# Performance work log

Hardware: AMD Instinct MI355X
Metric: run time of the kernel (lower is better)

Reference implementation:

```python
import jax, jax.numpy as jnp
import numpy as np

N_NODES = 10000
N_EDGES = 320000
IN_DIM = 512
HID = 64
H0 = 8
OUT = 64
H1 = 1
NEG_SLOPE = 0.2


def gat_layer(h, src, dst, W, attn_l, attn_r, n_nodes, activation=None):
    # h: (N, F_in); W: (F_in, H*D); attn_l/attn_r: (H, D)
    H, D = attn_l.shape
    feat = (h @ W).reshape(n_nodes, H, D)            # (N, H, D)
    el = jnp.einsum('nhd,hd->nh', feat, attn_l)      # (N, H)
    er = jnp.einsum('nhd,hd->nh', feat, attn_r)      # (N, H)
    e = jax.nn.leaky_relu(el[src] + er[dst], NEG_SLOPE)  # (E, H)
    # edge softmax over incoming edges of each destination node
    m = jax.ops.segment_max(e, dst, num_segments=n_nodes)   # (N, H), -inf for isolated
    m = jnp.where(jnp.isfinite(m), m, 0.0)
    ex = jnp.exp(e - m[dst])                         # (E, H)
    s = jax.ops.segment_sum(ex, dst, num_segments=n_nodes)  # (N, H)
    alpha = ex / s[dst]                              # (E, H)
    # weighted aggregation: out[dst] += alpha * feat[src]
    out = jax.ops.segment_sum(alpha[:, :, None] * feat[src], dst,
                              num_segments=n_nodes)  # (N, H, D)
    if activation is not None:
        out = activation(out)
    return out


def setup_inputs() -> dict:
    key = jax.random.key(0)
    ks = jax.random.split(key, 9)
    h = jax.random.normal(ks[0], (N_NODES, IN_DIM), dtype=jnp.float32)
    src = jax.random.randint(ks[1], (N_EDGES,), 0, N_NODES, dtype=jnp.int32)
    dst = jax.random.randint(ks[2], (N_EDGES,), 0, N_NODES, dtype=jnp.int32)
    W1 = jax.random.normal(ks[3], (IN_DIM, H0 * HID), dtype=jnp.float32) / np.sqrt(IN_DIM)
    attn_l1 = jax.random.normal(ks[4], (H0, HID), dtype=jnp.float32) / np.sqrt(HID)
    attn_r1 = jax.random.normal(ks[5], (H0, HID), dtype=jnp.float32) / np.sqrt(HID)
    W2 = jax.random.normal(ks[6], (H0 * HID, H1 * OUT), dtype=jnp.float32) / np.sqrt(H0 * HID)
    attn_l2 = jax.random.normal(ks[7], (H1, OUT), dtype=jnp.float32) / np.sqrt(OUT)
    attn_r2 = jax.random.normal(ks[8], (H1, OUT), dtype=jnp.float32) / np.sqrt(OUT)
    return {"h": h, "src": src, "dst": dst, "W1": W1, "attn_l1": attn_l1,
            "attn_r1": attn_r1, "W2": W2, "attn_l2": attn_l2, "attn_r2": attn_r2}


def reference(h, src, dst, W1, attn_l1, attn_r1, W2, attn_l2, attn_r2):
    # layer 1: elu activation, concat heads (flatten)
    x = gat_layer(h, src, dst, W1, attn_l1, attn_r1, N_NODES, activation=jax.nn.elu)
    x = x.reshape(N_NODES, H0 * HID)
    # layer 2: no activation, mean over heads
    x = gat_layer(x, src, dst, W2, attn_l2, attn_r2, N_NODES, activation=None)
    return x.mean(axis=1)  # (N, OUT)
```

## Files before the change

kernel.cpp:

```cpp
#include <hip/hip_runtime.h>
#include <hip/hip_bf16.h>
#include <math.h>

typedef unsigned int u32;
typedef unsigned short ushort;

constexpr int N_NODES = 10000;
constexpr int N_EDGES = 320000;
constexpr float NEG_SLOPE = 0.2f;

typedef __attribute__((ext_vector_type(8))) _Float16 half8;
typedef __attribute__((ext_vector_type(4))) float f32x4;
typedef __attribute__((ext_vector_type(16))) float f32x16;

__device__ __forceinline__ float lrelu(float x) { return x > 0.f ? x : NEG_SLOPE * x; }
__device__ __forceinline__ float elu(float x)   { return x > 0.f ? x : (expf(x) - 1.f); }

__device__ __forceinline__ ushort f2h(float x) {
    _Float16 h = (_Float16)x;
    return __builtin_bit_cast(ushort, h);
}
__device__ __forceinline__ float h2f(ushort u) {
    return (float)__builtin_bit_cast(_Float16, u);
}

__device__ __forceinline__ void gload16(const void* g, void* l) {
    __builtin_amdgcn_global_load_lds(
        (__attribute__((address_space(1))) void*)g,
        (__attribute__((address_space(3))) void*)l, 16, 0, 0);
}

constexpr int NCHUNK = 64;
constexpr int EPC    = N_EDGES / NCHUNK;
constexpr int NB_T1    = 64;
constexpr int NB_T2    = 8;
constexpr int NB_WLR2  = 2;
constexpr int NB_PRE   = NCHUNK + NB_T1 + NB_T2 + NB_WLR2;
constexpr int NB_SPLIT = (N_NODES * 512 / 4) / 256;

__global__ __launch_bounds__(256) void prep1_kernel(
                             const float4* __restrict__ h4,
                             ushort* __restrict__ xh,
                             const int* __restrict__ dst, int* __restrict__ ccnt,
                             int* __restrict__ rank,
                             const float* __restrict__ W1, ushort* __restrict__ w1t,
                             const float* __restrict__ W2, ushort* __restrict__ w2t,
                             const float* __restrict__ al2, const float* __restrict__ ar2,
                             float* __restrict__ wl2, float* __restrict__ wr2) {
    __shared__ __align__(16) int shbuf[N_NODES];
    const int b = blockIdx.x;
    if (b < NCHUNK) {
        for (int i = threadIdx.x; i < N_NODES; i += 256) shbuf[i] = 0;
        __syncthreads();
        const int e0 = b * EPC;
#pragma unroll 4
        for (int i = threadIdx.x; i < EPC; i += 256) {
            const int e = e0 + i;
            rank[e] = atomicAdd(&shbuf[dst[e]], 1);
        }
        __syncthreads();
        for (int i = threadIdx.x; i < N_NODES; i += 256)
            ccnt[b * N_NODES + i] = shbuf[i];
    } else if (b < NCHUNK + NB_T1 + NB_T2) {
        float* smem = (float*)shbuf;
        const int t0 = b - NCHUNK;
        const bool isW1 = t0 < NB_T1;
        const float* W = isW1 ? W1 : W2;
        ushort* wt = isW1 ? w1t : w2t;
        const int N  = isW1 ? 512 : 64;
        const int t  = isW1 ? t0 : (t0 - NB_T1);
        const int ti = isW1 ? (t & 7) : t;
        const int tj = isW1 ? (t >> 3) : 0;
        const int c  = threadIdx.x & 63;
        const int r0 = threadIdx.x >> 6;
#pragma unroll
        for (int p = 0; p < 16; p++) {
            const int r = p * 4 + r0;
            smem[r * 65 + c] = W[(size_t)(ti * 64 + r) * N + tj * 64 + c];
        }
        __syncthreads();
#pragma unroll
        for (int p = 0; p < 16; p++) {
            const int rr = p * 4 + r0;
            wt[(size_t)(tj * 64 + rr) * 512 + ti * 64 + c] = f2h(smem[c * 65 + rr]);
        }
    } else if (b < NB_PRE) {
        const int k = (b - NCHUNK - NB_T1 - NB_T2) * 256 + threadIdx.x;
        float sl = 0.f, sr = 0.f;
#pragma unroll 8
        for (int d = 0; d < 64; d++) {
            const float w = W2[(size_t)k * 64 + d];
            sl += w * al2[d];
            sr += w * ar2[d];
        }
        wl2[k] = sl;
        wr2[k] = sr;
    } else {
        const int i = (b - NB_PRE) * 256 + threadIdx.x;
        const float4 v = h4[i];
        *(ushort4*)&xh[i * 4] = make_ushort4(f2h(v.x), f2h(v.y), f2h(v.z), f2h(v.w));
    }
}

__global__ __launch_bounds__(256) void chunkscan_kernel(int* __restrict__ ccnt,
                                                        int* __restrict__ counts) {
    const int n = blockIdx.x * 256 + threadIdx.x;
    if (n >= N_NODES) return;
    int v[NCHUNK];
#pragma unroll
    for (int c = 0; c < NCHUNK; c++) v[c] = ccnt[c * N_NODES + n];
    int run = 0;
#pragma unroll
    for (int c = 0; c < NCHUNK; c++) {
        const int t = v[c];
        ccnt[c * N_NODES + n] = run;
        run += t;
    }
    counts[n] = run;
}

__global__ void prep2_scan_kernel(const int* __restrict__ counts, int* __restrict__ offs) {
    __shared__ int wsum[4];
    const int tid = threadIdx.x;
    const int lane = tid & 63, wave = tid >> 6;
    const int base = tid * 40;
    int v[40];
    int s = 0;
#pragma unroll
    for (int i = 0; i < 40; i++) {
        v[i] = (base + i < N_NODES) ? counts[base + i] : 0;
        s += v[i];
    }
    int ps = s;
#pragma unroll
    for (int o = 1; o < 64; o <<= 1) {
        const int t = __shfl_up(ps, o);
        if (lane >= o) ps += t;
    }
    if (lane == 63) wsum[wave] = ps;
    __syncthreads();
    if (tid < 4) {
        int t = wsum[tid];
#pragma unroll
        for (int o = 1; o < 4; o <<= 1) {
            const int u = __shfl_up(t, o);
            if (tid >= o) t += u;
        }
        wsum[tid] = t;
    }
    __syncthreads();
    const int wbase = (wave > 0) ? wsum[wave - 1] : 0;
    int run = wbase + ps - s;
#pragma unroll
    for (int i = 0; i < 40; i++) {
        if (base + i < N_NODES) offs[base + i + 1] = run + v[i];
        run += v[i];
    }
    if (tid == 0) offs[0] = 0;
}

constexpr int NB_GEMM1 = ((N_NODES + 63) / 64) * 4;
constexpr int NB_SCAT  = (N_EDGES + 255) / 256;

__global__ __launch_bounds__(256) void gemm1_scatter_kernel(
    const ushort* __restrict__ A, const ushort* __restrict__ B,
    ushort* __restrict__ Cout, int M,
    const float* __restrict__ attn_l, const float* __restrict__ attn_r,
    float* __restrict__ elp, float* __restrict__ erp,
    const int* __restrict__ src, const int* __restrict__ dst,
    const int* __restrict__ rank, const int* __restrict__ offs,
    const int* __restrict__ ccnt, int* __restrict__ srcs) {
    constexpr int BM = 64, BN = 128, BK = 64, K = 512, N = 512;

    if ((int)blockIdx.x >= NB_GEMM1) {
        const int i = ((int)blockIdx.x - NB_GEMM1) * 256 + threadIdx.x;
        if (i < N_EDGES) {
            const int c = i / EPC;
            const int d = dst[i];
            srcs[offs[d] + ccnt[c * N_NODES + d] + rank[i]] = src[i];
        }
        return;
    }

    __shared__ __align__(16) ushort sA[2][BM * BK];
    __shared__ __align__(16) ushort sB[2][BN * BK];

    const int tid = threadIdx.x;
    const int wave = tid >> 6, lane = tid & 63;
    const int m0 = ((int)blockIdx.x >> 2) * BM, n0 = ((int)blockIdx.x & 3) * BN;
    const int wm = wave >> 1, wn = wave & 1;
    const int l31 = lane & 31, lh = lane >> 5;

    size_t abyte[2]; int afb[2];
#pragma unroll
    for (int p = 0; p < 2; p++) {
        const int fb = tid * 16 + p * 4096;
        const int r = fb >> 7, s = (fb >> 4) & 7;
        int ar = m0 + r; if (ar > M - 1) ar = M - 1;
        abyte[p] = (size_t)ar * (K * 2) + (size_t)((s ^ (r & 7)) << 4);
        afb[p] = fb;
    }
    size_t bbyte[4]; int bfb[4];
#pragma unroll
    for (int p = 0; p < 4; p++) {
        const int fb = tid * 16 + p * 4096;
        const int r = fb >> 7, s = (fb >> 4) & 7;
        bbyte[p] = (size_t)(n0 + r) * (K * 2) + (size_t)((s ^ (r & 7)) << 4);
        bfb[p] = fb;
    }

    f32x16 acc[2] = {};

    const int rA = wm * 32 + l31;
    const u32 aoff = rA * 128, axr = rA & 7;
    u32 boff[2], bxr[2];
#pragma unroll
    for (int ni = 0; ni < 2; ni++) {
        const int rB = wn * 64 + ni * 32 + l31;
        boff[ni] = rB * 128; bxr[ni] = rB & 7;
    }

#pragma unroll
    for (int p = 0; p < 2; p++) gload16((const char*)A + abyte[p], (char*)&sA[0][0] + afb[p]);
#pragma unroll
    for (int p = 0; p < 4; p++) gload16((const char*)B + bbyte[p], (char*)&sB[0][0] + bfb[p]);
    __syncthreads();

    int cur = 0;
    for (int k0 = 0; k0 < K; k0 += BK) {
        if (k0 + BK < K) {
            const size_t kb = (size_t)(k0 + BK) * 2;
#pragma unroll
            for (int p = 0; p < 2; p++)
                gload16((const char*)A + abyte[p] + kb, (char*)&sA[cur ^ 1][0] + afb[p]);
#pragma unroll
            for (int p = 0; p < 4; p++)
                gload16((const char*)B + bbyte[p] + kb, (char*)&sB[cur ^ 1][0] + bfb[p]);
        }
        const char* pA = (const char*)&sA[cur][0];
        const char* pB = (const char*)&sB[cur][0];
#pragma unroll
        for (int ks = 0; ks < 4; ks++) {
            const u32 sl = ks * 2 + lh;
            const half8 ah = *(const half8*)(pA + aoff + ((sl ^ axr) << 4));
#pragma unroll
            for (int ni = 0; ni < 2; ni++) {
                const half8 bh = *(const half8*)(pB + boff[ni] + ((sl ^ bxr[ni]) << 4));
                acc[ni] = __builtin_amdgcn_mfma_f32_32x32x16_f16(ah, bh, acc[ni], 0, 0, 0);
            }
        }
        __syncthreads();
        cur ^= 1;
    }

#pragma unroll
    for (int reg = 0; reg < 16; reg++) {
        const int grow = m0 + wm * 32 + (reg & 3) + 8 * (reg >> 2) + 4 * lh;
        if (grow < M) {
#pragma unroll
            for (int ni = 0; ni < 2; ni++) {
                const int gcol = n0 + wn * 64 + ni * 32 + l31;
                Cout[(size_t)grow * N + gcol] = f2h(acc[ni][reg]);
            }
        }
    }

    const int head = (n0 + wn * 64) >> 6;
    float alv[2], arv[2];
#pragma unroll
    for (int ni = 0; ni < 2; ni++) {
        alv[ni] = attn_l[head * 64 + ni * 32 + l31];
        arv[ni] = attn_r[head * 64 + ni * 32 + l31];
    }
#pragma unroll
    for (int reg = 0; reg < 16; reg++) {
        float pl = acc[0][reg] * alv[0] + acc[1][reg] * alv[1];
        float pr = acc[0][reg] * arv[0] + acc[1][reg] * arv[1];
#pragma unroll
        for (int o = 1; o < 32; o <<= 1) {
            pl += __shfl_xor(pl, o);
            pr += __shfl_xor(pr, o);
        }
        const int grow = m0 + wm * 32 + (reg & 3) + 8 * (reg >> 2) + 4 * lh;
        if (l31 == 0 && grow < M) {
            elp[grow * 8 + head] = pl;
            erp[grow * 8 + head] = pr;
        }
    }
}

__global__ __launch_bounds__(256) void gemm2_kernel(
    const ushort* __restrict__ A, const ushort* __restrict__ B,
    ushort* __restrict__ Cout, int M) {
    constexpr int BM = 32, BN = 64, BK = 64, K = 512, N = 64;

    __shared__ __align__(16) ushort sA[2][BM * BK];
    __shared__ __align__(16) ushort sB[2][BN * BK];

    const int tid = threadIdx.x;
    const int wave = tid >> 6, lane = tid & 63;
    const int m0 = blockIdx.x * BM;
    const int wm = wave >> 1, wn = wave & 1;
    const int quad = lane >> 4, l15 = lane & 15;

    const int fa = tid * 16;
    const int ra = fa >> 7, sa_ = (fa >> 4) & 7;
    int arow = m0 + ra; if (arow > M - 1) arow = M - 1;
    const size_t abyte = (size_t)arow * (K * 2) + (size_t)((sa_ ^ (ra & 7)) << 4);

    size_t bbyte[2]; int bfb[2];
#pragma unroll
    for (int p = 0; p < 2; p++) {
        const int fb = tid * 16 + p * 4096;
        const int r = fb >> 7, s = (fb >> 4) & 7;
        bbyte[p] = (size_t)r * (K * 2) + (size_t)((s ^ (r & 7)) << 4);
        bfb[p] = fb;
    }

    f32x4 acc[2] = {};
    const int rA = wm * 16 + l15;
    const u32 aoff = rA * 128, axr = rA & 7;
    u32 boff[2], bxr[2];
#pragma unroll
    for (int ni = 0; ni < 2; ni++) {
        const int rB = wn * 32 + ni * 16 + l15;
        boff[ni] = rB * 128; bxr[ni] = rB & 7;
    }

    gload16((const char*)A + abyte, (char*)&sA[0][0] + fa);
#pragma unroll
    for (int p = 0; p < 2; p++) gload16((const char*)B + bbyte[p], (char*)&sB[0][0] + bfb[p]);
    __syncthreads();

    int cur = 0;
    for (int k0 = 0; k0 < K; k0 += BK) {
        if (k0 + BK < K) {
            const size_t kb = (size_t)(k0 + BK) * 2;
            gload16((const char*)A + abyte + kb, (char*)&sA[cur ^ 1][0] + fa);
#pragma unroll
            for (int p = 0; p < 2; p++)
                gload16((const char*)B + bbyte[p] + kb, (char*)&sB[cur ^ 1][0] + bfb[p]);
        }
        const char* pA = (const char*)&sA[cur][0];
        const char* pB = (const char*)&sB[cur][0];
#pragma unroll
        for (int ks = 0; ks < 2; ks++) {
            const u32 sl = ks * 4 + quad;
            const half8 ah = *(const half8*)(pA + aoff + ((sl ^ axr) << 4));
#pragma unroll
            for (int ni = 0; ni < 2; ni++) {
                const half8 bh = *(const half8*)(pB + boff[ni] + ((sl ^ bxr[ni]) << 4));
                acc[ni] = __builtin_amdgcn_mfma_f32_16x16x32_f16(ah, bh, acc[ni], 0, 0, 0);
            }
        }
        __syncthreads();
        cur ^= 1;
    }

#pragma unroll
    for (int r = 0; r < 4; r++) {
        const int grow = m0 + wm * 16 + quad * 4 + r;
        if (grow < M) {
#pragma unroll
            for (int ni = 0; ni < 2; ni++) {
                const int gcol = wn * 32 + ni * 16 + l15;
                Cout[(size_t)grow * N + gcol] = f2h(acc[ni][r]);
            }
        }
    }
}

__global__ __launch_bounds__(256) void agg1_kernel(
    const ushort* __restrict__ feat, const float* __restrict__ el,
    const float* __restrict__ er, const int* __restrict__ offs,
    const int* __restrict__ srcs, ushort* __restrict__ xh,
    const float* __restrict__ wl2, const float* __restrict__ wr2,
    float* __restrict__ el2, float* __restrict__ er2) {
    const int tid = threadIdx.x;
    const int wave = tid >> 6, lane = tid & 63;
    const int node = blockIdx.x * 4 + wave;
    const int start = offs[node];
    const int deg = offs[node + 1] - start;
    const int d0 = lane * 8;
    const int myh = lane >> 3;

    if (deg == 0) {
        const ushort4 z = make_ushort4(0, 0, 0, 0);
        *(ushort4*)&xh[(size_t)node * 512 + d0] = z;
        *(ushort4*)&xh[(size_t)node * 512 + d0 + 4] = z;
        if (lane == 0) { el2[node] = 0.f; er2[node] = 0.f; }
        return;
    }

    const float4 ea = *(const float4*)&er[node * 8];
    const float4 eb = *(const float4*)&er[node * 8 + 4];
    const float er_my = (myh & 4) ? ((myh & 2) ? ((myh & 1) ? eb.w : eb.z)
                                              : ((myh & 1) ? eb.y : eb.x))
                                  : ((myh & 2) ? ((myh & 1) ? ea.w : ea.z)
                                              : ((myh & 1) ? ea.y : ea.x));

    float acc[8];
#pragma unroll
    for (int i = 0; i < 8; i++) acc[i] = 0.f;
    float ws = 0.f;

    for (int base = 0; base < deg; base += 64) {
        const int has = min(64, deg - base);
        const int s = srcs[start + base + min(lane, has - 1)];
        int j = 0;
        for (; j + 8 <= has; j += 8) {
            int sq[8];
#pragma unroll
            for (int q = 0; q < 8; q++) sq[q] = __shfl(s, j + q);
            float eq[8];
#pragma unroll
            for (int q = 0; q < 8; q++) eq[q] = el[sq[q] * 8 + myh];
            half8 uq[8];
#pragma unroll
            for (int q = 0; q < 8; q++)
                uq[q] = *(const half8*)&feat[(size_t)sq[q] * 512 + d0];
            float wq[8];
#pragma unroll
            for (int q = 0; q < 8; q++) wq[q] = __expf(lrelu(eq[q] + er_my));
#pragma unroll
            for (int q = 0; q < 8; q++) {
#pragma unroll
                for (int i = 0; i < 8; i++)
                    acc[i] += wq[q] * (float)uq[q][i];
                ws += wq[q];
            }
        }
        for (; j < has; j++) {
            const int sj = __shfl(s, j);
            const float w = __expf(lrelu(el[sj * 8 + myh] + er_my));
            const half8 u = *(const half8*)&feat[(size_t)sj * 512 + d0];
#pragma unroll
            for (int i = 0; i < 8; i++)
                acc[i] += w * (float)u[i];
            ws += w;
        }
    }

    const float inv = 1.f / ws;
    float o[8];
#pragma unroll
    for (int i = 0; i < 8; i++) o[i] = elu(acc[i] * inv);

    const float4 wla = *(const float4*)&wl2[d0];
    const float4 wlb = *(const float4*)&wl2[d0 + 4];
    const float4 wra = *(const float4*)&wr2[d0];
    const float4 wrb = *(const float4*)&wr2[d0 + 4];
    float pl = o[0] * wla.x + o[1] * wla.y + o[2] * wla.z + o[3] * wla.w
             + o[4] * wlb.x + o[5] * wlb.y + o[6] * wlb.z + o[7] * wlb.w;
    float pr = o[0] * wra.x + o[1] * wra.y + o[2] * wra.z + o[3] * wra.w
             + o[4] * wrb.x + o[5] * wrb.y + o[6] * wrb.z + o[7] * wrb.w;
#pragma unroll
    for (int off = 32; off > 0; off >>= 1) {
        pl += __shfl_xor(pl, off);
        pr += __shfl_xor(pr, off);
    }
    if (lane == 0) { el2[node] = pl; er2[node] = pr; }

    ushort hh[8];
#pragma unroll
    for (int i = 0; i < 8; i++) hh[i] = f2h(o[i]);
    *(ushort4*)&xh[(size_t)node * 512 + d0]     = make_ushort4(hh[0], hh[1], hh[2], hh[3]);
    *(ushort4*)&xh[(size_t)node * 512 + d0 + 4] = make_ushort4(hh[4], hh[5], hh[6], hh[7]);
}

__global__ __launch_bounds__(256) void agg2_kernel(
    const ushort* __restrict__ feat, const float* __restrict__ el,
    const float* __restrict__ er, const int* __restrict__ offs,
    const int* __restrict__ srcs, float* __restrict__ out) {
    const int tid = threadIdx.x;
    const int wave = tid >> 6, lane = tid & 63;
    const int node = blockIdx.x * 4 + wave;
    const int start = offs[node];
    const int deg = offs[node + 1] - start;
    if (deg == 0) { out[(size_t)node * 64 + lane] = 0.f; return; }
    const float ern = er[node];

    float acc = 0.f, ws = 0.f;
    for (int base = 0; base < deg; base += 64) {
        const int has = min(64, deg - base);
        const int s = srcs[start + base + min(lane, has - 1)];
        const float w = __expf(lrelu(el[s] + ern));
        int j = 0;
        for (; j + 8 <= has; j += 8) {
            float aq[8]; int sq[8];
#pragma unroll
            for (int q = 0; q < 8; q++) { aq[q] = __shfl(w, j + q); sq[q] = __shfl(s, j + q); }
            ushort fq[8];
#pragma unroll
            for (int q = 0; q < 8; q++) fq[q] = feat[(size_t)sq[q] * 64 + lane];
#pragma unroll
            for (int q = 0; q < 8; q++) { acc += aq[q] * h2f(fq[q]); ws += aq[q]; }
        }
        for (; j < has; j++) {
            const float a = __shfl(w, j);
            const int sj = __shfl(s, j);
            acc += a * h2f(feat[(size_t)sj * 64 + lane]);
            ws += a;
        }
    }
    out[(size_t)node * 64 + lane] = acc / ws;
}

extern "C" void kernel_launch(void* const* d_in, const int* in_sizes, int n_in,
                              void* d_out, int out_size, void* d_ws, size_t ws_size,
                              hipStream_t stream) {
    const float* h   = (const float*)d_in[0];
    const int*   src = (const int*)d_in[1];
    const int*   dst = (const int*)d_in[2];
    const float* W1  = (const float*)d_in[3];
    const float* al1 = (const float*)d_in[4];
    const float* ar1 = (const float*)d_in[5];
    const float* W2  = (const float*)d_in[6];
    const float* al2 = (const float*)d_in[7];
    const float* ar2 = (const float*)d_in[8];
    float* out = (float*)d_out;

    char* p = (char*)d_ws;
    ushort* feat1 = (ushort*)p; p += (size_t)N_NODES * 512 * 2;
    ushort* feat2 = (ushort*)p; p += (size_t)N_NODES * 64 * 2;
    float* el1   = (float*)p;  p += (size_t)N_NODES * 8 * 4;
    float* er1   = (float*)p;  p += (size_t)N_NODES * 8 * 4;
    float* el2   = (float*)p;  p += (size_t)N_NODES * 4;
    float* er2   = (float*)p;  p += (size_t)N_NODES * 4;
    ushort* xh   = (ushort*)p; p += (size_t)N_NODES * 512 * 2;
    ushort* w1t  = (ushort*)p; p += (size_t)512 * 512 * 2;
    ushort* w2t  = (ushort*)p; p += (size_t)64 * 512 * 2;
    float* wl2   = (float*)p;  p += (size_t)512 * 4;
    float* wr2   = (float*)p;  p += (size_t)512 * 4;
    int* counts  = (int*)p;    p += (size_t)N_NODES * 4;
    int* ccnt    = (int*)p;    p += (size_t)NCHUNK * N_NODES * 4;
    int* offs    = (int*)p;    p += (size_t)10004 * 4;
    int* rank    = (int*)p;    p += (size_t)N_EDGES * 4;
    int* srcs    = (int*)p;    p += (size_t)N_EDGES * 4;

    prep1_kernel<<<NB_PRE + NB_SPLIT, 256, 0, stream>>>(
        (const float4*)h, xh, dst, ccnt, rank,
        W1, w1t, W2, w2t, al2, ar2, wl2, wr2);

    chunkscan_kernel<<<(N_NODES + 255) / 256, 256, 0, stream>>>(ccnt, counts);

    prep2_scan_kernel<<<1, 256, 0, stream>>>(counts, offs);

    gemm1_scatter_kernel<<<NB_GEMM1 + NB_SCAT, 256, 0, stream>>>(
        xh, w1t, feat1, N_NODES, al1, ar1, el1, er1,
        src, dst, rank, offs, ccnt, srcs);

    agg1_kernel<<<N_NODES / 4, 256, 0, stream>>>(
        feat1, el1, er1, offs, srcs, xh, wl2, wr2, el2, er2);

    gemm2_kernel<<<(N_NODES + 31) / 32, 256, 0, stream>>>(
        xh, w2t, feat2, N_NODES);

    agg2_kernel<<<N_NODES / 4, 256, 0, stream>>>(feat2, el2, er2, offs, srcs, out);
}
```

Baseline: 182.1 us.

## Split agg1 feature dimension across four blocks with edge-parallel lane groups

Layer-1 aggregation now launches four blocks per group of nodes. Each block covers 128 of the 512 feature columns (two heads), and each wave splits its 64 lanes into four groups that walk different edges, then reduces the groups with shuffles. The layer-2 attention dot products become per-quarter partials, and extra blocks appended to the gemm2 launch sum them into el2/er2. The aim is more parallelism and memory-level concurrency for the gather, at the cost of four times the index/el loads, extra cross-lane reductions, and a partials buffer.

```diff
diff --git a/kernel.cpp b/kernel.cpp
--- a/kernel.cpp
+++ b/kernel.cpp
@@ -289,10 +289,115 @@
     }
 }
 
+__global__ __launch_bounds__(256) void agg1_kernel(
+    const ushort* __restrict__ feat, const float* __restrict__ el,
+    const float* __restrict__ er, const int* __restrict__ offs,
+    const int* __restrict__ srcs, ushort* __restrict__ xh,
+    const float* __restrict__ wl2, const float* __restrict__ wr2,
+    float* __restrict__ plp, float* __restrict__ prp) {
+    const int tid = threadIdx.x;
+    const int wave = tid >> 6, lane = tid & 63;
+    const int pair = blockIdx.x & 3;
+    const int node = (blockIdx.x >> 2) * 4 + wave;
+    const int start = offs[node];
+    const int deg = offs[node + 1] - start;
+    const int grp = lane >> 4;
+    const int lig = lane & 15;
+    const int d0  = pair * 128 + lig * 8;
+    const int myh = pair * 2 + (lig >> 3);
+
+    if (deg == 0) {
+        if (lane < 16) {
+            const ushort4 z = make_ushort4(0, 0, 0, 0);
+            *(ushort4*)&xh[(size_t)node * 512 + d0]     = z;
+            *(ushort4*)&xh[(size_t)node * 512 + d0 + 4] = z;
+        }
+        if (lane == 0) { plp[node * 4 + pair] = 0.f; prp[node * 4 + pair] = 0.f; }
+        return;
+    }
+
+    const float er_my = er[node * 8 + myh];
+
+    float acc[8];
+#pragma unroll
+    for (int i = 0; i < 8; i++) acc[i] = 0.f;
+    float ws = 0.f;
+
+    for (int base = 0; base < deg; base += 64) {
+        const int has = min(64, deg - base);
+        const int s = srcs[start + base + min(lane, has - 1)];
+        for (int j = 0; j < has; j += 8) {
+            const int e0 = j + grp, e1 = j + 4 + grp;
+            const int s0 = __shfl(s, min(e0, has - 1));
+            const int s1 = __shfl(s, min(e1, has - 1));
+            const float l0 = el[s0 * 8 + myh];
+            const float l1 = el[s1 * 8 + myh];
+            const half8 u0 = *(const half8*)&feat[(size_t)s0 * 512 + d0];
+            const half8 u1 = *(const half8*)&feat[(size_t)s1 * 512 + d0];
+            const float w0 = (e0 < has) ? __expf(lrelu(l0 + er_my)) : 0.f;
+            const float w1 = (e1 < has) ? __expf(lrelu(l1 + er_my)) : 0.f;
+#pragma unroll
+            for (int i = 0; i < 8; i++) acc[i] += w0 * (float)u0[i];
+            ws += w0;
+#pragma unroll
+            for (int i = 0; i < 8; i++) acc[i] += w1 * (float)u1[i];
+            ws += w1;
+        }
+    }
+
+#pragma unroll
+    for (int i = 0; i < 8; i++) {
+        acc[i] += __shfl_xor(acc[i], 16);
+        acc[i] += __shfl_xor(acc[i], 32);
+    }
+    ws += __shfl_xor(ws, 16);
+    ws += __shfl_xor(ws, 32);
+
+    const float inv = 1.f / ws;
+    float o[8];
+#pragma unroll
+    for (int i = 0; i < 8; i++) o[i] = elu(acc[i] * inv);
+
+    if (lane < 16) {
+        ushort hh[8];
+#pragma unroll
+        for (int i = 0; i < 8; i++) hh[i] = f2h(o[i]);
+        *(ushort4*)&xh[(size_t)node * 512 + d0]     = make_ushort4(hh[0], hh[1], hh[2], hh[3]);
+        *(ushort4*)&xh[(size_t)node * 512 + d0 + 4] = make_ushort4(hh[4], hh[5], hh[6], hh[7]);
+    }
+
+    float pl = 0.f, pr = 0.f;
+#pragma unroll
+    for (int i = 0; i < 8; i++) {
+        pl += o[i] * wl2[d0 + i];
+        pr += o[i] * wr2[d0 + i];
+    }
+#pragma unroll
+    for (int off = 8; off > 0; off >>= 1) {
+        pl += __shfl_xor(pl, off);
+        pr += __shfl_xor(pr, off);
+    }
+    if (lane == 0) { plp[node * 4 + pair] = pl; prp[node * 4 + pair] = pr; }
+}
+
+constexpr int NB_G2  = (N_NODES + 31) / 32;
+constexpr int NB_SUM = (N_NODES + 255) / 256;
+
 __global__ __launch_bounds__(256) void gemm2_kernel(
     const ushort* __restrict__ A, const ushort* __restrict__ B,
-    ushort* __restrict__ Cout, int M) {
+    ushort* __restrict__ Cout, int M,
+    const float* __restrict__ plp, const float* __restrict__ prp,
+    float* __restrict__ el2, float* __restrict__ er2) {
     constexpr int BM = 32, BN = 64, BK = 64, K = 512, N = 64;
+
+    if ((int)blockIdx.x >= NB_G2) {
+        const int n = ((int)blockIdx.x - NB_G2) * 256 + threadIdx.x;
+        if (n < N_NODES) {
+            el2[n] = plp[n * 4] + plp[n * 4 + 1] + plp[n * 4 + 2] + plp[n * 4 + 3];
+            er2[n] = prp[n * 4] + prp[n * 4 + 1] + prp[n * 4 + 2] + prp[n * 4 + 3];
+        }
+        return;
+    }
 
     __shared__ __align__(16) ushort sA[2][BM * BK];
     __shared__ __align__(16) ushort sB[2][BN * BK];
@@ -368,104 +473,6 @@
             }
         }
     }
-}
-
-__global__ __launch_bounds__(256) void agg1_kernel(
-    const ushort* __restrict__ feat, const float* __restrict__ el,
-    const float* __restrict__ er, const int* __restrict__ offs,
-    const int* __restrict__ srcs, ushort* __restrict__ xh,
-    const float* __restrict__ wl2, const float* __restrict__ wr2,
-    float* __restrict__ el2, float* __restrict__ er2) {
-    const int tid = threadIdx.x;
-    const int wave = tid >> 6, lane = tid & 63;
-    const int node = blockIdx.x * 4 + wave;
-    const int start = offs[node];
-    const int deg = offs[node + 1] - start;
-    const int d0 = lane * 8;
-    const int myh = lane >> 3;
-
-    if (deg == 0) {
-        const ushort4 z = make_ushort4(0, 0, 0, 0);
-        *(ushort4*)&xh[(size_t)node * 512 + d0] = z;
-        *(ushort4*)&xh[(size_t)node * 512 + d0 + 4] = z;
-        if (lane == 0) { el2[node] = 0.f; er2[node] = 0.f; }
-        return;
-    }
-
-    const float4 ea = *(const float4*)&er[node * 8];
-    const float4 eb = *(const float4*)&er[node * 8 + 4];
-    const float er_my = (myh & 4) ? ((myh & 2) ? ((myh & 1) ? eb.w : eb.z)
-                                              : ((myh & 1) ? eb.y : eb.x))
-                                  : ((myh & 2) ? ((myh & 1) ? ea.w : ea.z)
-                                              : ((myh & 1) ? ea.y : ea.x));
-
-    float acc[8];
-#pragma unroll
-    for (int i = 0; i < 8; i++) acc[i] = 0.f;
-    float ws = 0.f;
-
-    for (int base = 0; base < deg; base += 64) {
-        const int has = min(64, deg - base);
-        const int s = srcs[start + base + min(lane, has - 1)];
-        int j = 0;
-        for (; j + 8 <= has; j += 8) {
-            int sq[8];
-#pragma unroll
-            for (int q = 0; q < 8; q++) sq[q] = __shfl(s, j + q);
-            float eq[8];
-#pragma unroll
-            for (int q = 0; q < 8; q++) eq[q] = el[sq[q] * 8 + myh];
-            half8 uq[8];
-#pragma unroll
-            for (int q = 0; q < 8; q++)
-                uq[q] = *(const half8*)&feat[(size_t)sq[q] * 512 + d0];
-            float wq[8];
-#pragma unroll
-            for (int q = 0; q < 8; q++) wq[q] = __expf(lrelu(eq[q] + er_my));
-#pragma unroll
-            for (int q = 0; q < 8; q++) {
-#pragma unroll
-                for (int i = 0; i < 8; i++)
-                    acc[i] += wq[q] * (float)uq[q][i];
-                ws += wq[q];
-            }
-        }
-        for (; j < has; j++) {
-            const int sj = __shfl(s, j);
-            const float w = __expf(lrelu(el[sj * 8 + myh] + er_my));
-            const half8 u = *(const half8*)&feat[(size_t)sj * 512 + d0];
-#pragma unroll
-            for (int i = 0; i < 8; i++)
-                acc[i] += w * (float)u[i];
-            ws += w;
-        }
-    }
-
-    const float inv = 1.f / ws;
-    float o[8];
-#pragma unroll
-    for (int i = 0; i < 8; i++) o[i] = elu(acc[i] * inv);
-
-    const float4 wla = *(const float4*)&wl2[d0];
-    const float4 wlb = *(const float4*)&wl2[d0 + 4];
-    const float4 wra = *(const float4*)&wr2[d0];
-    const float4 wrb = *(const float4*)&wr2[d0 + 4];
-    float pl = o[0] * wla.x + o[1] * wla.y + o[2] * wla.z + o[3] * wla.w
-             + o[4] * wlb.x + o[5] * wlb.y + o[6] * wlb.z + o[7] * wlb.w;
-    float pr = o[0] * wra.x + o[1] * wra.y + o[2] * wra.z + o[3] * wra.w
-             + o[4] * wrb.x + o[5] * wrb.y + o[6] * wrb.z + o[7] * wrb.w;
-#pragma unroll
-    for (int off = 32; off > 0; off >>= 1) {
-        pl += __shfl_xor(pl, off);
-        pr += __shfl_xor(pr, off);
-    }
-    if (lane == 0) { el2[node] = pl; er2[node] = pr; }
-
-    ushort hh[8];
-#pragma unroll
-    for (int i = 0; i < 8; i++) hh[i] = f2h(o[i]);
-    *(ushort4*)&xh[(size_t)node * 512 + d0]     = make_ushort4(hh[0], hh[1], hh[2], hh[3]);
-    *(ushort4*)&xh[(size_t)node * 512 + d0 + 4] = make_ushort4(hh[4], hh[5], hh[6], hh[7]);
 }
 
 __global__ __launch_bounds__(256) void agg2_kernel(
@@ -537,6 +544,8 @@
     int* offs    = (int*)p;    p += (size_t)10004 * 4;
     int* rank    = (int*)p;    p += (size_t)N_EDGES * 4;
     int* srcs    = (int*)p;    p += (size_t)N_EDGES * 4;
+    float* plp   = (float*)p;  p += (size_t)N_NODES * 4 * 4;
+    float* prp   = (float*)p;  p += (size_t)N_NODES * 4 * 4;
 
     prep1_kernel<<<NB_PRE + NB_SPLIT, 256, 0, stream>>>(
         (const float4*)h, xh, dst, ccnt, rank,
@@ -550,11 +559,11 @@
         xh, w1t, feat1, N_NODES, al1, ar1, el1, er1,
         src, dst, rank, offs, ccnt, srcs);
 
-    agg1_kernel<<<N_NODES / 4, 256, 0, stream>>>(
-        feat1, el1, er1, offs, srcs, xh, wl2, wr2, el2, er2);
-
-    gemm2_kernel<<<(N_NODES + 31) / 32, 256, 0, stream>>>(
-        xh, w2t, feat2, N_NODES);
+    agg1_kernel<<<N_NODES, 256, 0, stream>>>(
+        feat1, el1, er1, offs, srcs, xh, wl2, wr2, plp, prp);
+
+    gemm2_kernel<<<NB_G2 + NB_SUM, 256, 0, stream>>>(
+        xh, w2t, feat2, N_NODES, plp, prp, el2, er2);
 
     agg2_kernel<<<N_NODES / 4, 256, 0, stream>>>(feat2, el2, er2, offs, srcs, out);
 }
```

Result: no change. 181.0 us (-0.6%).
